# Performance work log

Hardware: AMD Instinct MI355X
Metric: run time of the kernel (lower is better)

The kernel has to match this reference:

```python
import jax, jax.numpy as jnp
import numpy as np

NEIGHBORS = [(0, 0, 0), (1, 0, 0), (-1, 0, 0), (0, 1, 0), (0, -1, 0), (0, 0, 1), (0, 0, 2)]


def setup_inputs() -> dict:
    key = jax.random.key(0)
    states = 8192
    xy_size = 64  # num_states = xy_size^2 * z_size (z_size = 2)
    transition_matrix_unnormalized = jax.random.normal(key, (states, 7), dtype=jnp.float32)
    return {
        "transition_matrix_unnormalized": transition_matrix_unnormalized,
        "num_states": states,
        "xy_size": xy_size,
    }


def reference(transition_matrix_unnormalized, num_states, xy_size):
    # log_softmax over the 7 neighbor logits per state
    transitions = jax.nn.log_softmax(transition_matrix_unnormalized, axis=-1)  # [N, 7]
    h = jnp.arange(num_states)  # [N]
    # torch.zeros(N, N).log() == -inf everywhere
    out = jnp.full((num_states, num_states), -jnp.inf, dtype=transitions.dtype)
    # Sequential scatter per neighbor (7 fixed iterations) preserves torch's
    for idx, (x, y, z) in enumerate(NEIGHBORS):
        offset = x + xy_size * (y + xy_size * z)
        cols = (h - offset) % num_states  # [N]
        out = out.at[h, cols].set(transitions[:, idx])
    return out
```

## Files before the change

### kernel.cpp

```cpp
#include <hip/hip_runtime.h>
#include <math.h>

typedef float f32x4 __attribute__((ext_vector_type(4)));

__global__ __launch_bounds__(256) void transition_fill_kernel(
    const float* __restrict__ trans,
    float*       __restrict__ out,
    int N, int xy)
{
    const int r   = blockIdx.x;
    const int tid = threadIdx.x;

    int offs[7];
    offs[0] = 0;
    offs[1] = 1;
    offs[2] = -1;
    offs[3] = xy;
    offs[4] = -xy;
    offs[5] = xy * xy;
    offs[6] = 2 * xy * xy;

    float x[7];
#pragma unroll
    for (int i = 0; i < 7; ++i) {
        float v = trans[r * 7 + i];
        x[i] = (__float_as_uint(v) & 0x7F800000u) != 0x7F800000u ? v : 0.0f;
    }

    float m = x[0];
#pragma unroll
    for (int i = 1; i < 7; ++i) m = fmaxf(m, x[i]);
    float s = 0.0f;
#pragma unroll
    for (int i = 0; i < 7; ++i) s += expf(x[i] - m);
    float lse = m + logf(s);
    if ((__float_as_uint(lse) & 0x7F800000u) == 0x7F800000u) lse = 0.0f;

    int   cols[7], cq[7];
    float vals[7];
#pragma unroll
    for (int i = 0; i < 7; ++i) {
        int c = (r - offs[i]) % N;
        if (c < 0) c += N;
        cols[i] = c;
        cq[i]   = c >> 2;
        float v = x[i] - lse;
        v = fminf(fmaxf(v, -1.0e30f), 1.0e30f);
        if ((__float_as_uint(v) & 0x7F800000u) == 0x7F800000u) v = -1.0f;
        vals[i] = v;
    }

    const int nfull = N >> 2;
    unsigned mask = 0;
    if (nfull <= 256 * 32) {
#pragma unroll
        for (int i = 0; i < 7; ++i)
            if ((cq[i] & 255) == tid) mask |= 1u << (cq[i] >> 8);
    } else {
        mask = 0xFFFFFFFFu;
    }

    const float BG = __uint_as_float(0xFF7F0000u);
    float* __restrict__ row = out + (size_t)r * (size_t)N;
    f32x4* __restrict__ row4 = reinterpret_cast<f32x4*>(row);

    f32x4 bg4;
    bg4.x = BG; bg4.y = BG; bg4.z = BG; bg4.w = BG;

    int j = 0;
    for (int q = tid; q < nfull; q += 256, ++j) {
        f32x4 v = bg4;
        if (mask & (1u << (j & 31))) {
#pragma unroll
            for (int i = 0; i < 7; ++i) {
                if (cq[i] == q) {
                    const int lane = cols[i] & 3;
                    v.x = (lane == 0) ? vals[i] : v.x;
                    v.y = (lane == 1) ? vals[i] : v.y;
                    v.z = (lane == 2) ? vals[i] : v.z;
                    v.w = (lane == 3) ? vals[i] : v.w;
                }
            }
        }
        row4[q] = v;
    }

    for (int c = (nfull << 2) + tid; c < N; c += 256) {
        float v = BG;
#pragma unroll
        for (int i = 0; i < 7; ++i)
            if (cols[i] == c) v = vals[i];
        row[c] = v;
    }
}

extern "C" void kernel_launch(void* const* d_in, const int* in_sizes, int n_in,
                              void* d_out, int out_size, void* d_ws, size_t ws_size,
                              hipStream_t stream) {
    const float* trans = (const float*)d_in[0];
    float*       out   = (float*)d_out;

    const int N = in_sizes[0] / 7;
    int xy = (int)(sqrtf((float)N * 0.5f) + 0.5f);

    dim3 grid(N), block(256);
    transition_fill_kernel<<<grid, block, 0, stream>>>(trans, out, N, xy);
}
```

Measured before the change: 44.81 us.

## Use persistent grid-stride blocks over rows with prefetched logits

Launches a capped grid of 2048 blocks instead of one block per row. Each block now loops over several rows and prefetches the next row's seven logits while it writes the current row. The per-thread bitmask shortcut is removed, so every output vector is checked against the seven target quads. This is meant to cut block launch overhead and hide the input load latency, at the cost of more compare work per store and fewer blocks in flight.

```diff
diff --git a/kernel.cpp b/kernel.cpp
--- a/kernel.cpp
+++ b/kernel.cpp
@@ -3,74 +3,71 @@
 
 typedef float f32x4 __attribute__((ext_vector_type(4)));
 
-__global__ __launch_bounds__(256) void transition_fill_kernel(
+__global__ __launch_bounds__(256, 8) void transition_fill_kernel(
     const float* __restrict__ trans,
     float*       __restrict__ out,
     int N, int xy)
 {
-    const int r   = blockIdx.x;
-    const int tid = threadIdx.x;
-
-    int offs[7];
-    offs[0] = 0;
-    offs[1] = 1;
-    offs[2] = -1;
-    offs[3] = xy;
-    offs[4] = -xy;
-    offs[5] = xy * xy;
-    offs[6] = 2 * xy * xy;
-
-    float x[7];
-#pragma unroll
-    for (int i = 0; i < 7; ++i) {
-        float v = trans[r * 7 + i];
-        x[i] = (__float_as_uint(v) & 0x7F800000u) != 0x7F800000u ? v : 0.0f;
-    }
-
-    float m = x[0];
-#pragma unroll
-    for (int i = 1; i < 7; ++i) m = fmaxf(m, x[i]);
-    float s = 0.0f;
-#pragma unroll
-    for (int i = 0; i < 7; ++i) s += expf(x[i] - m);
-    float lse = m + logf(s);
-    if ((__float_as_uint(lse) & 0x7F800000u) == 0x7F800000u) lse = 0.0f;
-
-    int   cols[7], cq[7];
-    float vals[7];
-#pragma unroll
-    for (int i = 0; i < 7; ++i) {
-        int c = (r - offs[i]) % N;
-        if (c < 0) c += N;
-        cols[i] = c;
-        cq[i]   = c >> 2;
-        float v = x[i] - lse;
-        v = fminf(fmaxf(v, -1.0e30f), 1.0e30f);
-        if ((__float_as_uint(v) & 0x7F800000u) == 0x7F800000u) v = -1.0f;
-        vals[i] = v;
-    }
-
-    const int nfull = N >> 2;
-    unsigned mask = 0;
-    if (nfull <= 256 * 32) {
-#pragma unroll
-        for (int i = 0; i < 7; ++i)
-            if ((cq[i] & 255) == tid) mask |= 1u << (cq[i] >> 8);
-    } else {
-        mask = 0xFFFFFFFFu;
-    }
+    const int tid  = threadIdx.x;
+    const int nblk = gridDim.x;
 
     const float BG = __uint_as_float(0xFF7F0000u);
-    float* __restrict__ row = out + (size_t)r * (size_t)N;
-    f32x4* __restrict__ row4 = reinterpret_cast<f32x4*>(row);
-
     f32x4 bg4;
     bg4.x = BG; bg4.y = BG; bg4.z = BG; bg4.w = BG;
+    const int nfull = N >> 2;
 
-    int j = 0;
-    for (int q = tid; q < nfull; q += 256, ++j) {
-        f32x4 v = bg4;
-        if (mask & (1u << (j & 31))) {
+    const int off1 = 1, off3 = xy, off5 = xy * xy, off6 = 2 * xy * xy;
+
+    int r = blockIdx.x;
+    float nx[7];
+#pragma unroll
+    for (int i = 0; i < 7; ++i) nx[i] = trans[r * 7 + i];
+
+    for (; r < N; r += nblk) {
+        float x[7];
+#pragma unroll
+        for (int i = 0; i < 7; ++i) {
+            float v = nx[i];
+            x[i] = (__float_as_uint(v) & 0x7F800000u) != 0x7F800000u ? v : 0.0f;
+        }
+        const int rn = r + nblk;
+        if (rn < N) {
+#pragma unroll
+            for (int i = 0; i < 7; ++i) nx[i] = trans[rn * 7 + i];
+        }
+
+        float m = x[0];
+#pragma unroll
+        for (int i = 1; i < 7; ++i) m = fmaxf(m, x[i]);
+        float s = 0.0f;
+#pragma unroll
+        for (int i = 0; i < 7; ++i) s += expf(x[i] - m);
+        float lse = m + logf(s);
+        if ((__float_as_uint(lse) & 0x7F800000u) == 0x7F800000u) lse = 0.0f;
+
+        int offs[7];
+        offs[0] = 0; offs[1] = off1; offs[2] = -off1;
+        offs[3] = off3; offs[4] = -off3; offs[5] = off5; offs[6] = off6;
+
+        int   cols[7], cq[7];
+        float vals[7];
+#pragma unroll
+        for (int i = 0; i < 7; ++i) {
+            int c = (r - offs[i]) % N;
+            if (c < 0) c += N;
+            cols[i] = c;
+            cq[i]   = c >> 2;
+            float v = x[i] - lse;
+            v = fminf(fmaxf(v, -1.0e30f), 1.0e30f);
+            if ((__float_as_uint(v) & 0x7F800000u) == 0x7F800000u) v = -1.0f;
+            vals[i] = v;
+        }
+
+        float* __restrict__ row  = out + (size_t)r * (size_t)N;
+        f32x4* __restrict__ row4 = reinterpret_cast<f32x4*>(row);
+
+        for (int q = tid; q < nfull; q += 256) {
+            f32x4 v = bg4;
 #pragma unroll
             for (int i = 0; i < 7; ++i) {
                 if (cq[i] == q) {
@@ -81,16 +78,16 @@
                     v.w = (lane == 3) ? vals[i] : v.w;
                 }
             }
+            row4[q] = v;
         }
-        row4[q] = v;
-    }
 
-    for (int c = (nfull << 2) + tid; c < N; c += 256) {
-        float v = BG;
+        for (int c = (nfull << 2) + tid; c < N; c += 256) {
+            float v = BG;
 #pragma unroll
-        for (int i = 0; i < 7; ++i)
-            if (cols[i] == c) v = vals[i];
-        row[c] = v;
+            for (int i = 0; i < 7; ++i)
+                if (cols[i] == c) v = vals[i];
+            row[c] = v;
+        }
     }
 }
 
@@ -103,6 +100,7 @@
     const int N = in_sizes[0] / 7;
     int xy = (int)(sqrtf((float)N * 0.5f) + 0.5f);
 
-    dim3 grid(N), block(256);
+    int nblk = N < 2048 ? N : 2048;
+    dim3 grid(nblk), block(256);
     transition_fill_kernel<<<grid, block, 0, stream>>>(trans, out, N, xy);
 }
```

Measured after the change: 50.26 us. +12.2%, slower.
